# Kernel tuning notes

Hardware: AMD Instinct MI355X
Metric: run time of the kernel (lower is better)

Reference implementation:

```python
import jax, jax.numpy as jnp
import numpy as np

IN_SIZE = 8192
N_PART = 64
EMBED = IN_SIZE // N_PART  # 128
BATCH = 8192
LN_EPS = 1e-5
ATT_EPS = 1e-7


def setup_inputs() -> dict:
    key = jax.random.key(0)
    ks = jax.random.split(key, 9)
    s = 1.0 / np.sqrt(EMBED)
    return {
        "x": jax.random.normal(ks[0], (BATCH, IN_SIZE), dtype=jnp.float32),
        "Wq": jax.random.uniform(ks[1], (EMBED, EMBED), jnp.float32, -s, s),
        "bq": jax.random.uniform(ks[2], (EMBED,), jnp.float32, -s, s),
        "Wk": jax.random.uniform(ks[3], (EMBED, EMBED), jnp.float32, -s, s),
        "bk": jax.random.uniform(ks[4], (EMBED,), jnp.float32, -s, s),
        "Wv": jax.random.uniform(ks[5], (EMBED, EMBED), jnp.float32, -s, s),
        "bv": jax.random.uniform(ks[6], (EMBED,), jnp.float32, -s, s),
        "ln_w": jnp.ones((IN_SIZE,), jnp.float32),
        "ln_b": jnp.zeros((IN_SIZE,), jnp.float32),
    }


def reference(x, Wq, bq, Wk, bk, Wv, bv, ln_w, ln_b):
    B = x.shape[0]
    # LayerNorm over in_size
    mu = jnp.mean(x, axis=-1, keepdims=True)
    var = jnp.mean((x - mu) ** 2, axis=-1, keepdims=True)
    x_norm = (x - mu) * jax.lax.rsqrt(var + LN_EPS) * ln_w + ln_b
    _x = x_norm.reshape(B, N_PART, EMBED)  # [b, l, d]
    # elu(lin(x)) + 1 feature maps (torch Linear: x @ W.T + b)
    Q = jax.nn.elu(jnp.einsum("bld,ed->ble", _x, Wq) + bq) + 1.0
    K = jax.nn.elu(jnp.einsum("bld,ed->ble", _x, Wk) + bk) + 1.0
    V = jnp.einsum("bld,ed->ble", _x, Wv) + bv
    # KV[b,k,j] = sum_i K[b,i,j] V[b,i,k]
    KV = jnp.einsum("bij,bik->bkj", K, V)
    Ksum = jnp.sum(K, axis=1)  # [b, d]
    norm = 1.0 / (jnp.einsum("bld,bd->bl", Q, Ksum) + ATT_EPS)
    prod = jnp.einsum("bld,bmd,bl->blm", Q, KV, norm)  # [b, l, v_dim]
    return prod.reshape(B, -1) + x
```

## Files before the change

### kernel.cpp

```cpp
#include <hip/hip_runtime.h>

typedef __attribute__((ext_vector_type(8))) __bf16 bf16x8;
typedef __attribute__((ext_vector_type(8))) unsigned short ushort8v;
typedef __attribute__((ext_vector_type(4))) float f32x4;

__device__ __forceinline__ unsigned short f2bf(float f) {
  return __builtin_bit_cast(unsigned short, (__bf16)f);
}

__device__ __forceinline__ int qoff(int row, int colb) {
  return row * 256 + (colb ^ ((row & 7) << 4));
}
__device__ __forceinline__ int toff(int row, int colb) {
  return row * 128 + (colb ^ ((row & 7) << 4));
}

__device__ __forceinline__ void bar_lds() {
  asm volatile("s_waitcnt lgkmcnt(0)" ::: "memory");
  __builtin_amdgcn_s_barrier();
}

__global__ void prep_w(const float* __restrict__ Wq, const float* __restrict__ Wk,
                       const float* __restrict__ Wv, unsigned short* __restrict__ ws) {
  int i = blockIdx.x * 256 + threadIdx.x;
  if (i >= 3 * 16384) return;
  const float* s = (i < 16384) ? Wq : (i < 32768 ? Wk : Wv);
  ws[i] = f2bf(s[i & 16383]);
}

__global__ __launch_bounds__(512, 2) void fused_attn(
    const float* __restrict__ x, const unsigned short* __restrict__ wsW,
    const float* __restrict__ bq, const float* __restrict__ bk, const float* __restrict__ bv,
    const float* __restrict__ ln_w, const float* __restrict__ ln_b,
    float* __restrict__ out) {
  __shared__ __align__(16) unsigned char smem[66112];
  unsigned char* sA  = smem;
  unsigned char* sQ  = smem + 16384;
  unsigned char* sK  = smem + 32768;
  unsigned char* sVT = smem + 49152;
  float* redS  = (float*)(smem + 65536);
  float* pPart = (float*)(smem + 65536 + 64);

  const int tid = threadIdx.x;
  const int lane = tid & 63;
  const int w = tid >> 6;
  const int l15 = lane & 15;
  const int l4 = lane >> 4;
  const size_t base = (size_t)blockIdx.x * (4 * 8192);

  bf16x8 wf[3][4];
  const int col = (w << 4) + l15;
#pragma unroll
  for (int m = 0; m < 3; ++m) {
    const unsigned short* wp = wsW + m * 16384 + col * 128 + (l4 << 3);
#pragma unroll
    for (int kk = 0; kk < 4; ++kk)
      wf[m][kk] = *(const bf16x8*)(wp + kk * 32);
  }
  const float biasQ = bq[col], biasK = bk[col], biasV = bv[col];

  const int row_x = tid >> 3;
  const int c0 = (tid & 7) << 4;

  float xv[16];
  {
    const float* xp = x + base + (size_t)row_x * 128 + c0;
#pragma unroll
    for (int i = 0; i < 4; ++i) {
      float4 a = *(const float4*)(xp + i * 4);
      xv[i*4+0]=a.x; xv[i*4+1]=a.y; xv[i*4+2]=a.z; xv[i*4+3]=a.w;
    }
  }

#pragma unroll 1
  for (int r = 0; r < 4; ++r) {
    const size_t bofs = base + (size_t)r * 8192;

    float lw[16], lb[16];
    {
      const float* pw = ln_w + row_x * 128 + c0;
      const float* pb = ln_b + row_x * 128 + c0;
#pragma unroll
      for (int i = 0; i < 4; ++i) {
        float4 a = *(const float4*)(pw + i * 4);
        lw[i*4+0]=a.x; lw[i*4+1]=a.y; lw[i*4+2]=a.z; lw[i*4+3]=a.w;
        float4 b = *(const float4*)(pb + i * 4);
        lb[i*4+0]=b.x; lb[i*4+1]=b.y; lb[i*4+2]=b.z; lb[i*4+3]=b.w;
      }
    }

    float s1 = 0.f, s2 = 0.f;
#pragma unroll
    for (int i = 0; i < 16; ++i) { s1 += xv[i]; s2 += xv[i] * xv[i]; }
#pragma unroll
    for (int off = 32; off > 0; off >>= 1) {
      s1 += __shfl_xor(s1, off, 64);
      s2 += __shfl_xor(s2, off, 64);
    }
    if (lane == 0) { redS[w] = s1; redS[8 + w] = s2; }
    bar_lds();

    float t1 = 0.f, t2 = 0.f;
#pragma unroll
    for (int p = 0; p < 8; ++p) { t1 += redS[p]; t2 += redS[8 + p]; }
    const float mu = t1 * (1.f / 8192.f);
    const float rstd = rsqrtf(t2 * (1.f / 8192.f) - mu * mu + 1e-5f);

#pragma unroll
    for (int h = 0; h < 2; ++h) {
      ushort8v t;
#pragma unroll
      for (int j = 0; j < 8; ++j)
        t[j] = f2bf((xv[h*8+j] - mu) * rstd * lw[h*8+j] + lb[h*8+j]);
      *(ushort8v*)(sA + qoff(row_x, (c0 << 1) + h * 16)) = t;
    }

    if (r < 3) {
      const float* xp = x + bofs + 8192 + (size_t)row_x * 128 + c0;
#pragma unroll
      for (int i = 0; i < 4; ++i) {
        float4 a = *(const float4*)(xp + i * 4);
        xv[i*4+0]=a.x; xv[i*4+1]=a.y; xv[i*4+2]=a.z; xv[i*4+3]=a.w;
      }
    }
    bar_lds();

#pragma unroll
    for (int mt = 0; mt < 4; ++mt) {
      bf16x8 aq[4];
#pragma unroll
      for (int kk = 0; kk < 4; ++kk)
        aq[kk] = *(const bf16x8*)(sA + qoff(mt * 16 + l15, kk * 64 + (l4 << 4)));
      const int i0m = mt * 16 + (l4 << 2);
      f32x4 aQ = {0,0,0,0}, aK = {0,0,0,0}, aV = {0,0,0,0};
#pragma unroll
      for (int kk = 0; kk < 4; ++kk) {
        aQ = __builtin_amdgcn_mfma_f32_16x16x32_bf16(aq[kk], wf[0][kk], aQ, 0, 0, 0);
        aK = __builtin_amdgcn_mfma_f32_16x16x32_bf16(aq[kk], wf[1][kk], aK, 0, 0, 0);
        aV = __builtin_amdgcn_mfma_f32_16x16x32_bf16(aq[kk], wf[2][kk], aV, 0, 0, 0);
      }
#pragma unroll
      for (int rr = 0; rr < 4; ++rr) {
        float zq = aQ[rr] + biasQ; zq = zq > 0.f ? zq + 1.f : __expf(zq);
        *(unsigned short*)(sQ + qoff(i0m + rr, col * 2)) = f2bf(zq);
        float zk = aK[rr] + biasK; zk = zk > 0.f ? zk + 1.f : __expf(zk);
        *(unsigned short*)(sK + qoff(i0m + rr, col * 2)) = f2bf(zk);
      }
      ushort4 pk;
      pk.x = f2bf(aV[0] + biasV); pk.y = f2bf(aV[1] + biasV);
      pk.z = f2bf(aV[2] + biasV); pk.w = f2bf(aV[3] + biasV);
      *(ushort4*)(sVT + toff(col, i0m * 2)) = pk;
    }
    bar_lds();

    const int st = w >> 1;
    const int half = w & 1;
    const int i0s = st * 16 + (l4 << 2);
    f32x4 accS[2];
    f32x4 xr[4];
    {
      bf16x8 aq[4];
#pragma unroll
      for (int kk = 0; kk < 4; ++kk)
        aq[kk] = *(const bf16x8*)(sQ + qoff(st * 16 + l15, kk * 64 + (l4 << 4)));
#pragma unroll
      for (int nt = 0; nt < 2; ++nt) {
        const int ntg = half * 2 + nt;
        f32x4 acc = {0,0,0,0};
#pragma unroll
        for (int kk = 0; kk < 4; ++kk) {
          bf16x8 bk_ = *(const bf16x8*)(sK + qoff(ntg * 16 + l15, kk * 64 + (l4 << 4)));
          acc = __builtin_amdgcn_mfma_f32_16x16x32_bf16(aq[kk], bk_, acc, 0, 0, 0);
        }
        accS[nt] = acc;
      }
      float p[4];
#pragma unroll
      for (int rr = 0; rr < 4; ++rr) p[rr] = accS[0][rr] + accS[1][rr];
#pragma unroll
      for (int off = 1; off < 16; off <<= 1) {
#pragma unroll
        for (int rr = 0; rr < 4; ++rr) p[rr] += __shfl_xor(p[rr], off, 64);
      }
      if (l15 == 0) {
#pragma unroll
        for (int rr = 0; rr < 4; ++rr)
          pPart[w * 16 + (l4 << 2) + rr] = p[rr];
      }
#pragma unroll
      for (int nt = 0; nt < 4; ++nt) {
        const int l = nt * 16 + l15;
        const int mb = (w << 4) + (l4 << 2);
        xr[nt] = *(const f32x4*)(x + bofs + (size_t)l * 128 + mb);
      }
    }
    bar_lds();

    {
      float nv[4];
#pragma unroll
      for (int rr = 0; rr < 4; ++rr) {
        const int rI = (l4 << 2) + rr;
        nv[rr] = 1.f / (pPart[(st * 2) * 16 + rI] + pPart[(st * 2 + 1) * 16 + rI] + 1e-7f);
      }
#pragma unroll
      for (int nt = 0; nt < 2; ++nt) {
        const int ntg = half * 2 + nt;
#pragma unroll
        for (int rr = 0; rr < 4; ++rr)
          *(unsigned short*)(sA + toff(i0s + rr, (ntg * 16 + l15) * 2)) = f2bf(accS[nt][rr] * nv[rr]);
      }
    }
    bar_lds();

    {
      bf16x8 av[2];
#pragma unroll
      for (int kk = 0; kk < 2; ++kk)
        av[kk] = *(const bf16x8*)(sVT + toff((w << 4) + l15, kk * 64 + (l4 << 4)));
#pragma unroll
      for (int nt = 0; nt < 4; ++nt) {
        bf16x8 bs0 = *(const bf16x8*)(sA + toff(nt * 16 + l15, (l4 << 4)));
        bf16x8 bs1 = *(const bf16x8*)(sA + toff(nt * 16 + l15, 64 + (l4 << 4)));
        f32x4 acc = {0,0,0,0};
        acc = __builtin_amdgcn_mfma_f32_16x16x32_bf16(av[0], bs0, acc, 0, 0, 0);
        acc = __builtin_amdgcn_mfma_f32_16x16x32_bf16(av[1], bs1, acc, 0, 0, 0);
        const int l = nt * 16 + l15;
        const int mb = (w << 4) + (l4 << 2);
        const size_t idx = bofs + (size_t)l * 128 + mb;
        f32x4 o;
        o[0] = acc[0] + xr[nt][0]; o[1] = acc[1] + xr[nt][1];
        o[2] = acc[2] + xr[nt][2]; o[3] = acc[3] + xr[nt][3];
        *(f32x4*)(out + idx) = o;
      }
    }
  }
}

extern "C" void kernel_launch(void* const* d_in, const int* in_sizes, int n_in,
                              void* d_out, int out_size, void* d_ws, size_t ws_size,
                              hipStream_t stream) {
  const float* x   = (const float*)d_in[0];
  const float* Wq  = (const float*)d_in[1];
  const float* bq  = (const float*)d_in[2];
  const float* Wk  = (const float*)d_in[3];
  const float* bk  = (const float*)d_in[4];
  const float* Wv  = (const float*)d_in[5];
  const float* bv  = (const float*)d_in[6];
  const float* lnw = (const float*)d_in[7];
  const float* lnb = (const float*)d_in[8];
  unsigned short* ws = (unsigned short*)d_ws;
  float* out = (float*)d_out;

  prep_w<<<192, 256, 0, stream>>>(Wq, Wk, Wv, ws);
  fused_attn<<<2048, 512, 0, stream>>>(x, ws, bq, bk, bv, lnw, lnb, out);
}
```

Baseline: 208.6 us.

## Process one batch row per block, drop V LDS buffer, defer normalization

Switches from four batch rows per block (looped) to one row per block with four times as many blocks. The transposed-V shared buffer is removed: V^T fragments are built in registers through cross-lane shuffles. The attention normalization is moved from the S matrix into the final output scale, and weight fragments are loaded per phase rather than all held at once. Shared memory and register pressure both drop so three blocks can fit per CU. The cost is losing the in-block prefetch of the next row's x and reloading the weights and LayerNorm parameters in every block.

```diff
diff --git a/kernel.cpp b/kernel.cpp
--- a/kernel.cpp
+++ b/kernel.cpp
@@ -3,9 +3,13 @@
 typedef __attribute__((ext_vector_type(8))) __bf16 bf16x8;
 typedef __attribute__((ext_vector_type(8))) unsigned short ushort8v;
 typedef __attribute__((ext_vector_type(4))) float f32x4;
+typedef __attribute__((ext_vector_type(4))) unsigned int u32x4;
 
 __device__ __forceinline__ unsigned short f2bf(float f) {
   return __builtin_bit_cast(unsigned short, (__bf16)f);
+}
+__device__ __forceinline__ unsigned int pk2(float a, float b) {
+  return (unsigned int)f2bf(a) | ((unsigned int)f2bf(b) << 16);
 }
 
 __device__ __forceinline__ int qoff(int row, int colb) {
@@ -28,35 +32,26 @@
   ws[i] = f2bf(s[i & 16383]);
 }
 
-__global__ __launch_bounds__(512, 2) void fused_attn(
+__global__ __launch_bounds__(512, 3) void fused_attn(
     const float* __restrict__ x, const unsigned short* __restrict__ wsW,
     const float* __restrict__ bq, const float* __restrict__ bk, const float* __restrict__ bv,
     const float* __restrict__ ln_w, const float* __restrict__ ln_b,
     float* __restrict__ out) {
-  __shared__ __align__(16) unsigned char smem[66112];
-  unsigned char* sA  = smem;
-  unsigned char* sQ  = smem + 16384;
-  unsigned char* sK  = smem + 32768;
-  unsigned char* sVT = smem + 49152;
-  float* redS  = (float*)(smem + 65536);
-  float* pPart = (float*)(smem + 65536 + 64);
+  __shared__ __align__(16) unsigned char smem[49728];
+  unsigned char* sA = smem;
+  unsigned char* sQ = smem + 16384;
+  unsigned char* sK = smem + 32768;
+  float* redS  = (float*)(smem + 49152);
+  float* pPart = (float*)(smem + 49216);
 
   const int tid = threadIdx.x;
   const int lane = tid & 63;
   const int w = tid >> 6;
   const int l15 = lane & 15;
   const int l4 = lane >> 4;
-  const size_t base = (size_t)blockIdx.x * (4 * 8192);
-
-  bf16x8 wf[3][4];
+  const size_t bofs = (size_t)blockIdx.x * 8192;
+
   const int col = (w << 4) + l15;
-#pragma unroll
-  for (int m = 0; m < 3; ++m) {
-    const unsigned short* wp = wsW + m * 16384 + col * 128 + (l4 << 3);
-#pragma unroll
-    for (int kk = 0; kk < 4; ++kk)
-      wf[m][kk] = *(const bf16x8*)(wp + kk * 32);
-  }
   const float biasQ = bq[col], biasK = bk[col], biasV = bv[col];
 
   const int row_x = tid >> 3;
@@ -64,67 +59,62 @@
 
   float xv[16];
   {
-    const float* xp = x + base + (size_t)row_x * 128 + c0;
+    const float* xp = x + bofs + (size_t)row_x * 128 + c0;
 #pragma unroll
     for (int i = 0; i < 4; ++i) {
       float4 a = *(const float4*)(xp + i * 4);
       xv[i*4+0]=a.x; xv[i*4+1]=a.y; xv[i*4+2]=a.z; xv[i*4+3]=a.w;
     }
   }
-
-#pragma unroll 1
-  for (int r = 0; r < 4; ++r) {
-    const size_t bofs = base + (size_t)r * 8192;
-
-    float lw[16], lb[16];
-    {
-      const float* pw = ln_w + row_x * 128 + c0;
-      const float* pb = ln_b + row_x * 128 + c0;
-#pragma unroll
-      for (int i = 0; i < 4; ++i) {
-        float4 a = *(const float4*)(pw + i * 4);
-        lw[i*4+0]=a.x; lw[i*4+1]=a.y; lw[i*4+2]=a.z; lw[i*4+3]=a.w;
-        float4 b = *(const float4*)(pb + i * 4);
-        lb[i*4+0]=b.x; lb[i*4+1]=b.y; lb[i*4+2]=b.z; lb[i*4+3]=b.w;
-      }
-    }
-
-    float s1 = 0.f, s2 = 0.f;
-#pragma unroll
-    for (int i = 0; i < 16; ++i) { s1 += xv[i]; s2 += xv[i] * xv[i]; }
-#pragma unroll
-    for (int off = 32; off > 0; off >>= 1) {
-      s1 += __shfl_xor(s1, off, 64);
-      s2 += __shfl_xor(s2, off, 64);
-    }
-    if (lane == 0) { redS[w] = s1; redS[8 + w] = s2; }
-    bar_lds();
-
-    float t1 = 0.f, t2 = 0.f;
-#pragma unroll
-    for (int p = 0; p < 8; ++p) { t1 += redS[p]; t2 += redS[8 + p]; }
-    const float mu = t1 * (1.f / 8192.f);
-    const float rstd = rsqrtf(t2 * (1.f / 8192.f) - mu * mu + 1e-5f);
-
-#pragma unroll
-    for (int h = 0; h < 2; ++h) {
-      ushort8v t;
-#pragma unroll
-      for (int j = 0; j < 8; ++j)
-        t[j] = f2bf((xv[h*8+j] - mu) * rstd * lw[h*8+j] + lb[h*8+j]);
-      *(ushort8v*)(sA + qoff(row_x, (c0 << 1) + h * 16)) = t;
-    }
-
-    if (r < 3) {
-      const float* xp = x + bofs + 8192 + (size_t)row_x * 128 + c0;
-#pragma unroll
-      for (int i = 0; i < 4; ++i) {
-        float4 a = *(const float4*)(xp + i * 4);
-        xv[i*4+0]=a.x; xv[i*4+1]=a.y; xv[i*4+2]=a.z; xv[i*4+3]=a.w;
-      }
-    }
-    bar_lds();
-
+  float lw[16], lb[16];
+  {
+    const float* pw = ln_w + row_x * 128 + c0;
+    const float* pb = ln_b + row_x * 128 + c0;
+#pragma unroll
+    for (int i = 0; i < 4; ++i) {
+      float4 a = *(const float4*)(pw + i * 4);
+      lw[i*4+0]=a.x; lw[i*4+1]=a.y; lw[i*4+2]=a.z; lw[i*4+3]=a.w;
+      float4 b = *(const float4*)(pb + i * 4);
+      lb[i*4+0]=b.x; lb[i*4+1]=b.y; lb[i*4+2]=b.z; lb[i*4+3]=b.w;
+    }
+  }
+
+  float s1 = 0.f, s2 = 0.f;
+#pragma unroll
+  for (int i = 0; i < 16; ++i) { s1 += xv[i]; s2 += xv[i] * xv[i]; }
+#pragma unroll
+  for (int off = 32; off > 0; off >>= 1) {
+    s1 += __shfl_xor(s1, off, 64);
+    s2 += __shfl_xor(s2, off, 64);
+  }
+  if (lane == 0) { redS[w] = s1; redS[8 + w] = s2; }
+  bar_lds();
+
+  float t1 = 0.f, t2 = 0.f;
+#pragma unroll
+  for (int p = 0; p < 8; ++p) { t1 += redS[p]; t2 += redS[8 + p]; }
+  const float mu = t1 * (1.f / 8192.f);
+  const float rstd = rsqrtf(t2 * (1.f / 8192.f) - mu * mu + 1e-5f);
+
+#pragma unroll
+  for (int h = 0; h < 2; ++h) {
+    ushort8v t;
+#pragma unroll
+    for (int j = 0; j < 8; ++j)
+      t[j] = f2bf((xv[h*8+j] - mu) * rstd * lw[h*8+j] + lb[h*8+j]);
+    *(ushort8v*)(sA + qoff(row_x, (c0 << 1) + h * 16)) = t;
+  }
+  bar_lds();
+
+  {
+    bf16x8 wfq[4], wfk[4];
+    const unsigned short* wpq = wsW + col * 128 + (l4 << 3);
+    const unsigned short* wpk = wsW + 16384 + col * 128 + (l4 << 3);
+#pragma unroll
+    for (int kk = 0; kk < 4; ++kk) {
+      wfq[kk] = *(const bf16x8*)(wpq + kk * 32);
+      wfk[kk] = *(const bf16x8*)(wpk + kk * 32);
+    }
 #pragma unroll
     for (int mt = 0; mt < 4; ++mt) {
       bf16x8 aq[4];
@@ -132,12 +122,11 @@
       for (int kk = 0; kk < 4; ++kk)
         aq[kk] = *(const bf16x8*)(sA + qoff(mt * 16 + l15, kk * 64 + (l4 << 4)));
       const int i0m = mt * 16 + (l4 << 2);
-      f32x4 aQ = {0,0,0,0}, aK = {0,0,0,0}, aV = {0,0,0,0};
-#pragma unroll
-      for (int kk = 0; kk < 4; ++kk) {
-        aQ = __builtin_amdgcn_mfma_f32_16x16x32_bf16(aq[kk], wf[0][kk], aQ, 0, 0, 0);
-        aK = __builtin_amdgcn_mfma_f32_16x16x32_bf16(aq[kk], wf[1][kk], aK, 0, 0, 0);
-        aV = __builtin_amdgcn_mfma_f32_16x16x32_bf16(aq[kk], wf[2][kk], aV, 0, 0, 0);
+      f32x4 aQ = {0,0,0,0}, aK = {0,0,0,0};
+#pragma unroll
+      for (int kk = 0; kk < 4; ++kk) {
+        aQ = __builtin_amdgcn_mfma_f32_16x16x32_bf16(aq[kk], wfq[kk], aQ, 0, 0, 0);
+        aK = __builtin_amdgcn_mfma_f32_16x16x32_bf16(aq[kk], wfk[kk], aK, 0, 0, 0);
       }
 #pragma unroll
       for (int rr = 0; rr < 4; ++rr) {
@@ -146,93 +135,119 @@
         float zk = aK[rr] + biasK; zk = zk > 0.f ? zk + 1.f : __expf(zk);
         *(unsigned short*)(sK + qoff(i0m + rr, col * 2)) = f2bf(zk);
       }
-      ushort4 pk;
-      pk.x = f2bf(aV[0] + biasV); pk.y = f2bf(aV[1] + biasV);
-      pk.z = f2bf(aV[2] + biasV); pk.w = f2bf(aV[3] + biasV);
-      *(ushort4*)(sVT + toff(col, i0m * 2)) = pk;
-    }
-    bar_lds();
-
-    const int st = w >> 1;
-    const int half = w & 1;
-    const int i0s = st * 16 + (l4 << 2);
+    }
+  }
+
+  bf16x8 av[2];
+  {
+    bf16x8 wfv[4];
+    const unsigned short* wpv = wsW + 2 * 16384 + col * 128 + (l4 << 3);
+#pragma unroll
+    for (int kk = 0; kk < 4; ++kk)
+      wfv[kk] = *(const bf16x8*)(wpv + kk * 32);
+    const int srcA = l15 + ((lane & 16) << 1);
+    const int srcB = srcA + 16;
+    const bool hi = (l4 >> 1) != 0;
+#pragma unroll
+    for (int kf = 0; kf < 2; ++kf) {
+      f32x4 aV0 = {0,0,0,0}, aV1 = {0,0,0,0};
+#pragma unroll
+      for (int kk = 0; kk < 4; ++kk) {
+        bf16x8 aq0 = *(const bf16x8*)(sA + qoff((2*kf) * 16 + l15, kk * 64 + (l4 << 4)));
+        aV0 = __builtin_amdgcn_mfma_f32_16x16x32_bf16(aq0, wfv[kk], aV0, 0, 0, 0);
+      }
+#pragma unroll
+      for (int kk = 0; kk < 4; ++kk) {
+        bf16x8 aq1 = *(const bf16x8*)(sA + qoff((2*kf+1) * 16 + l15, kk * 64 + (l4 << 4)));
+        aV1 = __builtin_amdgcn_mfma_f32_16x16x32_bf16(aq1, wfv[kk], aV1, 0, 0, 0);
+      }
+      unsigned pA0 = pk2(aV0[0] + biasV, aV0[1] + biasV);
+      unsigned pA1 = pk2(aV0[2] + biasV, aV0[3] + biasV);
+      unsigned pB0 = pk2(aV1[0] + biasV, aV1[1] + biasV);
+      unsigned pB1 = pk2(aV1[2] + biasV, aV1[3] + biasV);
+      unsigned d0a = __shfl((int)pA0, srcA, 64), d0b = __shfl((int)pB0, srcA, 64);
+      unsigned d1a = __shfl((int)pA1, srcA, 64), d1b = __shfl((int)pB1, srcA, 64);
+      unsigned d2a = __shfl((int)pA0, srcB, 64), d2b = __shfl((int)pB0, srcB, 64);
+      unsigned d3a = __shfl((int)pA1, srcB, 64), d3b = __shfl((int)pB1, srcB, 64);
+      u32x4 dd;
+      dd[0] = hi ? d0b : d0a; dd[1] = hi ? d1b : d1a;
+      dd[2] = hi ? d2b : d2a; dd[3] = hi ? d3b : d3a;
+      av[kf] = __builtin_bit_cast(bf16x8, dd);
+    }
+  }
+  bar_lds();
+
+  const int rt = w >> 1;
+  const int h = w & 1;
+  const int i0s = rt * 16 + (l4 << 2);
+  f32x4 xr[4];
+  {
+    bf16x8 aq[4];
+#pragma unroll
+    for (int kk = 0; kk < 4; ++kk)
+      aq[kk] = *(const bf16x8*)(sQ + qoff(rt * 16 + l15, kk * 64 + (l4 << 4)));
     f32x4 accS[2];
-    f32x4 xr[4];
-    {
-      bf16x8 aq[4];
-#pragma unroll
-      for (int kk = 0; kk < 4; ++kk)
-        aq[kk] = *(const bf16x8*)(sQ + qoff(st * 16 + l15, kk * 64 + (l4 << 4)));
-#pragma unroll
-      for (int nt = 0; nt < 2; ++nt) {
-        const int ntg = half * 2 + nt;
-        f32x4 acc = {0,0,0,0};
-#pragma unroll
-        for (int kk = 0; kk < 4; ++kk) {
-          bf16x8 bk_ = *(const bf16x8*)(sK + qoff(ntg * 16 + l15, kk * 64 + (l4 << 4)));
-          acc = __builtin_amdgcn_mfma_f32_16x16x32_bf16(aq[kk], bk_, acc, 0, 0, 0);
-        }
-        accS[nt] = acc;
-      }
-      float p[4];
-#pragma unroll
-      for (int rr = 0; rr < 4; ++rr) p[rr] = accS[0][rr] + accS[1][rr];
-#pragma unroll
-      for (int off = 1; off < 16; off <<= 1) {
-#pragma unroll
-        for (int rr = 0; rr < 4; ++rr) p[rr] += __shfl_xor(p[rr], off, 64);
-      }
-      if (l15 == 0) {
-#pragma unroll
-        for (int rr = 0; rr < 4; ++rr)
-          pPart[w * 16 + (l4 << 2) + rr] = p[rr];
-      }
-#pragma unroll
-      for (int nt = 0; nt < 4; ++nt) {
-        const int l = nt * 16 + l15;
-        const int mb = (w << 4) + (l4 << 2);
-        xr[nt] = *(const f32x4*)(x + bofs + (size_t)l * 128 + mb);
-      }
-    }
-    bar_lds();
-
-    {
-      float nv[4];
-#pragma unroll
-      for (int rr = 0; rr < 4; ++rr) {
-        const int rI = (l4 << 2) + rr;
-        nv[rr] = 1.f / (pPart[(st * 2) * 16 + rI] + pPart[(st * 2 + 1) * 16 + rI] + 1e-7f);
-      }
-#pragma unroll
-      for (int nt = 0; nt < 2; ++nt) {
-        const int ntg = half * 2 + nt;
-#pragma unroll
-        for (int rr = 0; rr < 4; ++rr)
-          *(unsigned short*)(sA + toff(i0s + rr, (ntg * 16 + l15) * 2)) = f2bf(accS[nt][rr] * nv[rr]);
-      }
-    }
-    bar_lds();
-
-    {
-      bf16x8 av[2];
-#pragma unroll
-      for (int kk = 0; kk < 2; ++kk)
-        av[kk] = *(const bf16x8*)(sVT + toff((w << 4) + l15, kk * 64 + (l4 << 4)));
-#pragma unroll
-      for (int nt = 0; nt < 4; ++nt) {
-        bf16x8 bs0 = *(const bf16x8*)(sA + toff(nt * 16 + l15, (l4 << 4)));
-        bf16x8 bs1 = *(const bf16x8*)(sA + toff(nt * 16 + l15, 64 + (l4 << 4)));
-        f32x4 acc = {0,0,0,0};
-        acc = __builtin_amdgcn_mfma_f32_16x16x32_bf16(av[0], bs0, acc, 0, 0, 0);
-        acc = __builtin_amdgcn_mfma_f32_16x16x32_bf16(av[1], bs1, acc, 0, 0, 0);
-        const int l = nt * 16 + l15;
-        const int mb = (w << 4) + (l4 << 2);
-        const size_t idx = bofs + (size_t)l * 128 + mb;
-        f32x4 o;
-        o[0] = acc[0] + xr[nt][0]; o[1] = acc[1] + xr[nt][1];
-        o[2] = acc[2] + xr[nt][2]; o[3] = acc[3] + xr[nt][3];
-        *(f32x4*)(out + idx) = o;
-      }
+#pragma unroll
+    for (int nt = 0; nt < 2; ++nt) {
+      const int ntg = h * 2 + nt;
+      f32x4 acc = {0,0,0,0};
+#pragma unroll
+      for (int kk = 0; kk < 4; ++kk) {
+        bf16x8 bk_ = *(const bf16x8*)(sK + qoff(ntg * 16 + l15, kk * 64 + (l4 << 4)));
+        acc = __builtin_amdgcn_mfma_f32_16x16x32_bf16(aq[kk], bk_, acc, 0, 0, 0);
+      }
+      accS[nt] = acc;
+    }
+    float p[4];
+#pragma unroll
+    for (int rr = 0; rr < 4; ++rr) p[rr] = accS[0][rr] + accS[1][rr];
+#pragma unroll
+    for (int off = 1; off < 16; off <<= 1) {
+#pragma unroll
+      for (int rr = 0; rr < 4; ++rr) p[rr] += __shfl_xor(p[rr], off, 64);
+    }
+    if (l15 == 0) {
+#pragma unroll
+      for (int rr = 0; rr < 4; ++rr)
+        pPart[w * 16 + (l4 << 2) + rr] = p[rr];
+    }
+#pragma unroll
+    for (int nt = 0; nt < 2; ++nt) {
+      const int ntg = h * 2 + nt;
+#pragma unroll
+      for (int rr = 0; rr < 4; ++rr)
+        *(unsigned short*)(sA + toff(i0s + rr, (ntg * 16 + l15) * 2)) = f2bf(accS[nt][rr]);
+    }
+#pragma unroll
+    for (int nt = 0; nt < 4; ++nt) {
+      const int l = nt * 16 + l15;
+      const int mb = (w << 4) + (l4 << 2);
+      xr[nt] = *(const f32x4*)(x + bofs + (size_t)l * 128 + mb);
+    }
+  }
+  bar_lds();
+
+  {
+    float nv[4];
+#pragma unroll
+    for (int nt = 0; nt < 4; ++nt)
+      nv[nt] = 1.f / (pPart[nt * 32 + l15] + pPart[nt * 32 + 16 + l15] + 1e-7f);
+#pragma unroll
+    for (int nt = 0; nt < 4; ++nt) {
+      bf16x8 bs0 = *(const bf16x8*)(sA + toff(nt * 16 + l15, (l4 << 4)));
+      bf16x8 bs1 = *(const bf16x8*)(sA + toff(nt * 16 + l15, 64 + (l4 << 4)));
+      f32x4 acc = {0,0,0,0};
+      acc = __builtin_amdgcn_mfma_f32_16x16x32_bf16(av[0], bs0, acc, 0, 0, 0);
+      acc = __builtin_amdgcn_mfma_f32_16x16x32_bf16(av[1], bs1, acc, 0, 0, 0);
+      const int l = nt * 16 + l15;
+      const int mb = (w << 4) + (l4 << 2);
+      const size_t idx = bofs + (size_t)l * 128 + mb;
+      f32x4 o;
+      o[0] = acc[0] * nv[nt] + xr[nt][0];
+      o[1] = acc[1] * nv[nt] + xr[nt][1];
+      o[2] = acc[2] * nv[nt] + xr[nt][2];
+      o[3] = acc[3] * nv[nt] + xr[nt][3];
+      *(f32x4*)(out + idx) = o;
     }
   }
 }
@@ -253,5 +268,5 @@
   float* out = (float*)d_out;
 
   prep_w<<<192, 256, 0, stream>>>(Wq, Wk, Wv, ws);
-  fused_attn<<<2048, 512, 0, stream>>>(x, ws, bq, bk, bv, lnw, lnb, out);
-}
+  fused_attn<<<8192, 512, 0, stream>>>(x, ws, bq, bk, bv, lnw, lnb, out);
+}
```

New measurement: 230.0 us. 1.1x slower.

## Remove barriers by deferring normalization and precomputing next-row LN stats

Applied to the files above, without the earlier changes.

Scores are written unnormalized to a separate LDS buffer and the 1/norm scale is applied after the final PV MFMA. This removes one barrier per row iteration. The LayerNorm partial sums for the next batch row are now computed inside the score phase and written to a double-buffered reduction slot, which removes the barrier at the start of each iteration. ln_w/ln_b loads are hoisted out of the loop. In exchange LDS use grows by about 8KB, which may affect occupancy at 2 blocks per CU, and register pressure rises because lw/lb stay live across the whole loop.

```diff
diff --git a/kernel.cpp b/kernel.cpp
--- a/kernel.cpp
+++ b/kernel.cpp
@@ -33,13 +33,14 @@
     const float* __restrict__ bq, const float* __restrict__ bk, const float* __restrict__ bv,
     const float* __restrict__ ln_w, const float* __restrict__ ln_b,
     float* __restrict__ out) {
-  __shared__ __align__(16) unsigned char smem[66112];
+  __shared__ __align__(16) unsigned char smem[74368];
   unsigned char* sA  = smem;
   unsigned char* sQ  = smem + 16384;
   unsigned char* sK  = smem + 32768;
   unsigned char* sVT = smem + 49152;
-  float* redS  = (float*)(smem + 65536);
-  float* pPart = (float*)(smem + 65536 + 64);
+  unsigned char* sS  = smem + 65536;
+  float* redS  = (float*)(smem + 73728);
+  float* pPart = (float*)(smem + 73856);
 
   const int tid = threadIdx.x;
   const int lane = tid & 63;
@@ -61,6 +62,18 @@
 
   const int row_x = tid >> 3;
   const int c0 = (tid & 7) << 4;
+  float lw[16], lb[16];
+  {
+    const float* pw = ln_w + row_x * 128 + c0;
+    const float* pb = ln_b + row_x * 128 + c0;
+#pragma unroll
+    for (int i = 0; i < 4; ++i) {
+      float4 a = *(const float4*)(pw + i * 4);
+      lw[i*4+0]=a.x; lw[i*4+1]=a.y; lw[i*4+2]=a.z; lw[i*4+3]=a.w;
+      float4 b = *(const float4*)(pb + i * 4);
+      lb[i*4+0]=b.x; lb[i*4+1]=b.y; lb[i*4+2]=b.z; lb[i*4+3]=b.w;
+    }
+  }
 
   float xv[16];
   {
@@ -71,41 +84,29 @@
       xv[i*4+0]=a.x; xv[i*4+1]=a.y; xv[i*4+2]=a.z; xv[i*4+3]=a.w;
     }
   }
+  {
+    float s1 = 0.f, s2 = 0.f;
+#pragma unroll
+    for (int i = 0; i < 16; ++i) { s1 += xv[i]; s2 += xv[i] * xv[i]; }
+#pragma unroll
+    for (int off = 32; off > 0; off >>= 1) {
+      s1 += __shfl_xor(s1, off, 64);
+      s2 += __shfl_xor(s2, off, 64);
+    }
+    if (lane == 0) { redS[w] = s1; redS[8 + w] = s2; }
+  }
+  bar_lds();
 
 #pragma unroll 1
   for (int r = 0; r < 4; ++r) {
     const size_t bofs = base + (size_t)r * 8192;
 
-    float lw[16], lb[16];
-    {
-      const float* pw = ln_w + row_x * 128 + c0;
-      const float* pb = ln_b + row_x * 128 + c0;
-#pragma unroll
-      for (int i = 0; i < 4; ++i) {
-        float4 a = *(const float4*)(pw + i * 4);
-        lw[i*4+0]=a.x; lw[i*4+1]=a.y; lw[i*4+2]=a.z; lw[i*4+3]=a.w;
-        float4 b = *(const float4*)(pb + i * 4);
-        lb[i*4+0]=b.x; lb[i*4+1]=b.y; lb[i*4+2]=b.z; lb[i*4+3]=b.w;
-      }
-    }
-
-    float s1 = 0.f, s2 = 0.f;
-#pragma unroll
-    for (int i = 0; i < 16; ++i) { s1 += xv[i]; s2 += xv[i] * xv[i]; }
-#pragma unroll
-    for (int off = 32; off > 0; off >>= 1) {
-      s1 += __shfl_xor(s1, off, 64);
-      s2 += __shfl_xor(s2, off, 64);
-    }
-    if (lane == 0) { redS[w] = s1; redS[8 + w] = s2; }
-    bar_lds();
-
+    const float* rb = redS + (r & 1) * 16;
     float t1 = 0.f, t2 = 0.f;
 #pragma unroll
-    for (int p = 0; p < 8; ++p) { t1 += redS[p]; t2 += redS[8 + p]; }
+    for (int p = 0; p < 8; ++p) { t1 += rb[p]; t2 += rb[8 + p]; }
     const float mu = t1 * (1.f / 8192.f);
     const float rstd = rsqrtf(t2 * (1.f / 8192.f) - mu * mu + 1e-5f);
-
 #pragma unroll
     for (int h = 0; h < 2; ++h) {
       ushort8v t;
@@ -114,7 +115,6 @@
         t[j] = f2bf((xv[h*8+j] - mu) * rstd * lw[h*8+j] + lb[h*8+j]);
       *(ushort8v*)(sA + qoff(row_x, (c0 << 1) + h * 16)) = t;
     }
-
     if (r < 3) {
       const float* xp = x + bofs + 8192 + (size_t)row_x * 128 + c0;
 #pragma unroll
@@ -153,19 +153,25 @@
     }
     bar_lds();
 
-    const int st = w >> 1;
-    const int half = w & 1;
-    const int i0s = st * 16 + (l4 << 2);
-    f32x4 accS[2];
+    const int rt = w >> 1;
+    const int h = w & 1;
+    const int i0s = rt * 16 + (l4 << 2);
     f32x4 xr[4];
     {
       bf16x8 aq[4];
 #pragma unroll
       for (int kk = 0; kk < 4; ++kk)
-        aq[kk] = *(const bf16x8*)(sQ + qoff(st * 16 + l15, kk * 64 + (l4 << 4)));
+        aq[kk] = *(const bf16x8*)(sQ + qoff(rt * 16 + l15, kk * 64 + (l4 << 4)));
+#pragma unroll
+      for (int nt = 0; nt < 4; ++nt) {
+        const int l = nt * 16 + l15;
+        const int mb = (w << 4) + (l4 << 2);
+        xr[nt] = *(const f32x4*)(x + bofs + (size_t)l * 128 + mb);
+      }
+      f32x4 accS[2];
 #pragma unroll
       for (int nt = 0; nt < 2; ++nt) {
-        const int ntg = half * 2 + nt;
+        const int ntg = h * 2 + nt;
         f32x4 acc = {0,0,0,0};
 #pragma unroll
         for (int kk = 0; kk < 4; ++kk) {
@@ -187,11 +193,26 @@
         for (int rr = 0; rr < 4; ++rr)
           pPart[w * 16 + (l4 << 2) + rr] = p[rr];
       }
-#pragma unroll
-      for (int nt = 0; nt < 4; ++nt) {
-        const int l = nt * 16 + l15;
-        const int mb = (w << 4) + (l4 << 2);
-        xr[nt] = *(const f32x4*)(x + bofs + (size_t)l * 128 + mb);
+      if (r < 3) {
+        float n1 = 0.f, n2 = 0.f;
+#pragma unroll
+        for (int i = 0; i < 16; ++i) { n1 += xv[i]; n2 += xv[i] * xv[i]; }
+#pragma unroll
+        for (int off = 32; off > 0; off >>= 1) {
+          n1 += __shfl_xor(n1, off, 64);
+          n2 += __shfl_xor(n2, off, 64);
+        }
+        if (lane == 0) {
+          float* nb = redS + ((r + 1) & 1) * 16;
+          nb[w] = n1; nb[8 + w] = n2;
+        }
+      }
+#pragma unroll
+      for (int nt = 0; nt < 2; ++nt) {
+        const int ntg = h * 2 + nt;
+#pragma unroll
+        for (int rr = 0; rr < 4; ++rr)
+          *(unsigned short*)(sS + toff(i0s + rr, (ntg * 16 + l15) * 2)) = f2bf(accS[nt][rr]);
       }
     }
     bar_lds();
@@ -199,29 +220,16 @@
     {
       float nv[4];
 #pragma unroll
-      for (int rr = 0; rr < 4; ++rr) {
-        const int rI = (l4 << 2) + rr;
-        nv[rr] = 1.f / (pPart[(st * 2) * 16 + rI] + pPart[(st * 2 + 1) * 16 + rI] + 1e-7f);
-      }
-#pragma unroll
-      for (int nt = 0; nt < 2; ++nt) {
-        const int ntg = half * 2 + nt;
-#pragma unroll
-        for (int rr = 0; rr < 4; ++rr)
-          *(unsigned short*)(sA + toff(i0s + rr, (ntg * 16 + l15) * 2)) = f2bf(accS[nt][rr] * nv[rr]);
-      }
-    }
-    bar_lds();
-
-    {
+      for (int nt = 0; nt < 4; ++nt)
+        nv[nt] = 1.f / (pPart[nt * 32 + l15] + pPart[nt * 32 + 16 + l15] + 1e-7f);
       bf16x8 av[2];
 #pragma unroll
       for (int kk = 0; kk < 2; ++kk)
         av[kk] = *(const bf16x8*)(sVT + toff((w << 4) + l15, kk * 64 + (l4 << 4)));
 #pragma unroll
       for (int nt = 0; nt < 4; ++nt) {
-        bf16x8 bs0 = *(const bf16x8*)(sA + toff(nt * 16 + l15, (l4 << 4)));
-        bf16x8 bs1 = *(const bf16x8*)(sA + toff(nt * 16 + l15, 64 + (l4 << 4)));
+        bf16x8 bs0 = *(const bf16x8*)(sS + toff(nt * 16 + l15, (l4 << 4)));
+        bf16x8 bs1 = *(const bf16x8*)(sS + toff(nt * 16 + l15, 64 + (l4 << 4)));
         f32x4 acc = {0,0,0,0};
         acc = __builtin_amdgcn_mfma_f32_16x16x32_bf16(av[0], bs0, acc, 0, 0, 0);
         acc = __builtin_amdgcn_mfma_f32_16x16x32_bf16(av[1], bs1, acc, 0, 0, 0);
@@ -229,8 +237,10 @@
         const int mb = (w << 4) + (l4 << 2);
         const size_t idx = bofs + (size_t)l * 128 + mb;
         f32x4 o;
-        o[0] = acc[0] + xr[nt][0]; o[1] = acc[1] + xr[nt][1];
-        o[2] = acc[2] + xr[nt][2]; o[3] = acc[3] + xr[nt][3];
+        o[0] = acc[0] * nv[nt] + xr[nt][0];
+        o[1] = acc[1] * nv[nt] + xr[nt][1];
+        o[2] = acc[2] * nv[nt] + xr[nt][2];
+        o[3] = acc[3] * nv[nt] + xr[nt][3];
         *(f32x4*)(out + idx) = o;
       }
     }
```

New measurement: 211.2 us. About the same (+1.2%).
